# Kernel optimization log

Hardware: AMD Instinct MI355X
Metric: run time of the kernel (lower is better)

The kernel has to match this reference:

```python
import jax, jax.numpy as jnp
import numpy as np

N, E, G = 50000, 200000, 2048
D, H, L = 256, 512, 12
NODE_IN, EDGE_IN = 173, 13


def _mlp3(h, W1, b1, W2, b2, W3, b3):
    # DMCG-style MLP: ReLU after every Linear (MLPwoLastAct is the no-final-act variant)
    h = jax.nn.relu(h @ W1 + b1)
    h = jax.nn.relu(h @ W2 + b2)
    return jax.nn.relu(h @ W3 + b3)


def setup_inputs() -> dict:
    key = jax.random.key(0)
    ks = iter(jax.random.split(key, 64))

    def lin(fi, fo, shape_prefix=()):
        return jax.random.normal(next(ks), shape_prefix + (fi, fo), jnp.float32) / np.sqrt(fi)

    inp = {}
    inp["x_raw"] = jax.random.normal(next(ks), (N, NODE_IN), jnp.float32)
    inp["edge_raw"] = jax.random.normal(next(ks), (E, EDGE_IN), jnp.float32)
    inp["u0"] = jnp.zeros((1, D), jnp.float32)  # self.global_init
    # node / edge feature encoders: [H, H, D]
    inp["enW1"], inp["enb1"] = lin(NODE_IN, H), jnp.zeros((H,), jnp.float32)
    inp["enW2"], inp["enb2"] = lin(H, H), jnp.zeros((H,), jnp.float32)
    inp["enW3"], inp["enb3"] = lin(H, D), jnp.zeros((D,), jnp.float32)
    inp["eeW1"], inp["eeb1"] = lin(EDGE_IN, H), jnp.zeros((H,), jnp.float32)
    inp["eeW2"], inp["eeb2"] = lin(H, H), jnp.zeros((H,), jnp.float32)
    inp["eeW3"], inp["eeb3"] = lin(H, D), jnp.zeros((D,), jnp.float32)
    # per-message-passing-step MetaLayer MLPs, stacked over L layers
    inp["eW1"], inp["eb1"] = lin(4 * D, H, (L,)), jnp.zeros((L, H), jnp.float32)
    inp["eW2"], inp["eb2"] = lin(H, H, (L,)), jnp.zeros((L, H), jnp.float32)
    inp["eW3"], inp["eb3"] = lin(H, D, (L,)), jnp.zeros((L, D), jnp.float32)
    inp["nW1"], inp["nb1"] = lin(4 * D, H, (L,)), jnp.zeros((L, H), jnp.float32)
    inp["nW2"], inp["nb2"] = lin(H, H, (L,)), jnp.zeros((L, H), jnp.float32)
    inp["nW3"], inp["nb3"] = lin(H, D, (L,)), jnp.zeros((L, D), jnp.float32)
    inp["gW1"], inp["gb1"] = lin(3 * D, H, (L,)), jnp.zeros((L, H), jnp.float32)
    inp["gW2"], inp["gb2"] = lin(H, H, (L,)), jnp.zeros((L, H), jnp.float32)
    inp["gW3"], inp["gb3"] = lin(H, D, (L,)), jnp.zeros((L, D), jnp.float32)
    # per-step position head MLPwoLastAct(D, [D, 3])
    inp["pW1"], inp["pb1"] = lin(D, D, (L,)), jnp.zeros((L, D), jnp.float32)
    inp["pW2"], inp["pb2"] = lin(D, 3, (L,)), jnp.zeros((L, 3), jnp.float32)
    # graph structure (int constants)
    inp["edge_index"] = jax.random.randint(next(ks), (2, E), 0, N, jnp.int32)
    inp["node_batch"] = jnp.sort(jax.random.randint(next(ks), (N,), 0, G, jnp.int32))
    return inp


def reference(x_raw, edge_raw, u0, enW1, enb1, enW2, enb2, enW3, enb3,
              eeW1, eeb1, eeW2, eeb2, eeW3, eeb3,
              eW1, eb1, eW2, eb2, eW3, eb3,
              nW1, nb1, nW2, nb2, nW3, nb3,
              gW1, gb1, gW2, gb2, gW3, gb3,
              pW1, pb1, pW2, pb2,
              edge_index, node_batch):
    src, dst = edge_index[0], edge_index[1]
    edge_batch = node_batch[src]

    x = _mlp3(x_raw, enW1, enb1, enW2, enb2, enW3, enb3)        # [N, D]
    e = _mlp3(edge_raw, eeW1, eeb1, eeW2, eeb2, eeW3, eeb3)     # [E, D]
    u = jnp.broadcast_to(u0, (G, u0.shape[-1]))                  # [G, D]
    pos = jnp.zeros((x.shape[0], 3), x.dtype)

    def step(carry, p):
        x, e, u, pos = carry
        (ew1, ebb1, ew2, ebb2, ew3, ebb3,
         nw1, nbb1, nw2, nbb2, nw3, nbb3,
         gw1, gbb1, gw2, gbb2, gw3, gbb3,
         pw1, pbb1, pw2, pbb2) = p
        # edge update: gather endpoints + graph global, MLP, residual
        e_in = jnp.concatenate([e, x[src], x[dst], u[edge_batch]], axis=-1)   # [E, 4D]
        e = e + _mlp3(e_in, ew1, ebb1, ew2, ebb2, ew3, ebb3)
        # node update: scatter-sum edges to endpoints
        sent = jax.ops.segment_sum(e, src, num_segments=N)
        recv = jax.ops.segment_sum(e, dst, num_segments=N)
        n_in = jnp.concatenate([x, sent, recv, u[node_batch]], axis=-1)       # [N, 4D]
        x = x + _mlp3(n_in, nw1, nbb1, nw2, nbb2, nw3, nbb3)
        # global update: sum-pool nodes and edges per graph
        gn = jax.ops.segment_sum(x, node_batch, num_segments=G)
        ge = jax.ops.segment_sum(e, edge_batch, num_segments=G)
        u = u + _mlp3(jnp.concatenate([u, gn, ge], axis=-1), gw1, gbb1, gw2, gbb2, gw3, gbb3)
        # per-step position head (MLPwoLastAct)
        pos = pos + (jax.nn.relu(x @ pw1 + pbb1) @ pw2 + pbb2)
        return (x, e, u, pos), None

    params = (eW1, eb1, eW2, eb2, eW3, eb3,
              nW1, nb1, nW2, nb2, nW3, nb3,
              gW1, gb1, gW2, gb2, gW3, gb3,
              pW1, pb1, pW2, pb2)
    (x, e, u, pos), _ = jax.lax.scan(step, (x, e, u, pos), params)
    return pos
```

## Files before the change

### kernel.cpp

```cpp
#include <hip/hip_runtime.h>
#include <hip/hip_bf16.h>
#include <cstdint>
#include <cstddef>

#define N_NODES 50000
#define N_EDGES 200000
#define N_GRAPH 2048
#define DD 256
#define HH 512
#define LL 12
#define NODE_IN_F 173
#define EDGE_IN_F 13

typedef __hip_bfloat16 bf16;
typedef __attribute__((ext_vector_type(8))) short short8;
typedef __attribute__((ext_vector_type(4))) float f32x4;
typedef __attribute__((ext_vector_type(4))) unsigned short us4;

__device__ __forceinline__ float bfbits2f(unsigned short u) {
    return __uint_as_float(((unsigned)u) << 16);
}
__device__ __forceinline__ unsigned short f2bfbits(float f) {
    bf16 h = __float2bfloat16(f);
    return __builtin_bit_cast(unsigned short, h);
}

__device__ __forceinline__ void gld16(const void* g, void* l) {
    __builtin_amdgcn_global_load_lds(
        (const __attribute__((address_space(1))) unsigned int*)g,
        (__attribute__((address_space(3))) unsigned int*)l, 16, 0, 0);
}

#define TBM 128
#define TBN 128

struct GMArgs {
    const bf16* A[4];
    const int*  idx[4];
    const bf16* whi[4];
    const bf16* wlo[4];
    int lda[4];
    int ldw[4];
    int Kp[4];
    int nparts;
    int M, N;
    const float* bias;
    const bf16* res;
    bf16* C;
    int relu;
};

__global__ __launch_bounds__(256)
void gemm_mfma(GMArgs g)
{
    __shared__ __align__(16) short As[3][TBM * 32];
    __shared__ __align__(16) short Bh[3][TBN * 32];
    __shared__ __align__(16) short Bl[3][TBN * 32];

    const int tid  = threadIdx.x;
    const int lane = tid & 63;
    const int wv   = tid >> 6;
    const int wm   = (wv >> 1) * 64;
    const int wn   = (wv & 1) * 64;
    const int quad = lane >> 4;
    const int l16  = lane & 15;
    const int rq   = lane >> 2;
    const int qq   = lane & 3;

    const int gx  = gridDim.x;
    const int nwg = gx * gridDim.y;
    int hw  = blockIdx.y * gx + blockIdx.x;
    int xcd = hw & 7, rk = hw >> 3;
    int q = nwg >> 3, r = nwg & 7;
    int lid = (xcd < r ? xcd * (q + 1) : r * (q + 1) + (xcd - r) * q) + rk;
    const int row0 = (lid / gx) * TBM;
    const int col0 = (lid % gx) * TBN;

    int steps[4]; int T = 0;
#pragma unroll
    for (int p = 0; p < 4; ++p) { steps[p] = (p < g.nparts) ? (g.Kp[p] >> 5) : 0; T += steps[p]; }

    f32x4 acc[4][4];
#pragma unroll
    for (int i = 0; i < 4; ++i)
#pragma unroll
        for (int j = 0; j < 4; ++j)
            acc[i][j] = (f32x4){0.f, 0.f, 0.f, 0.f};

    auto stage = [&](int t, int b) {
        int p = 0, tt = t;
        while (tt >= steps[p]) { tt -= steps[p]; ++p; }
        const int k0 = tt << 5;
        const short* Ap  = (const short*)g.A[p];
        const short* Whi = (const short*)g.whi[p];
        const short* Wlo = (const short*)g.wlo[p];
        const int* idx = g.idx[p];
        const int lda = g.lda[p];
        const int ldw = g.ldw[p];
        const int kcol = k0 + qq * 8;
#pragma unroll
        for (int s = 0; s < 2; ++s) {
            int r2 = wv * 32 + s * 16 + rq;
            int slab = (wv * 32 + s * 16) * 32;
            int grr = row0 + r2;
            int cr = grr < g.M ? grr : g.M - 1;
            int ar = idx ? idx[cr] : cr;
            gld16(Ap + (size_t)ar * lda + kcol, (short*)As[b] + slab);
            size_t wo = (size_t)(col0 + r2) * ldw + kcol;
            gld16(Whi + wo, (short*)Bh[b] + slab);
            gld16(Wlo + wo, (short*)Bl[b] + slab);
        }
    };

    stage(0, 0);
    if (T > 1) stage(1, 1);
    int cur = 0;
    for (int t = 0; t < T; ++t) {
        if (t + 1 < T) asm volatile("s_waitcnt vmcnt(6)" ::: "memory");
        else           asm volatile("s_waitcnt vmcnt(0)" ::: "memory");
        __builtin_amdgcn_s_barrier();
        asm volatile("" ::: "memory");
        if (t + 2 < T) stage(t + 2, cur + 2 >= 3 ? cur - 1 : cur + 2);

        short8 a[4], bh[4], bl[4];
#pragma unroll
        for (int i = 0; i < 4; ++i)
            a[i] = *(const short8*)&As[cur][(wm + i * 16 + l16) * 32 + quad * 8];
#pragma unroll
        for (int j = 0; j < 4; ++j) {
            bh[j] = *(const short8*)&Bh[cur][(wn + j * 16 + l16) * 32 + quad * 8];
            bl[j] = *(const short8*)&Bl[cur][(wn + j * 16 + l16) * 32 + quad * 8];
        }
#pragma unroll
        for (int i = 0; i < 4; ++i)
#pragma unroll
            for (int j = 0; j < 4; ++j)
                acc[i][j] = __builtin_amdgcn_mfma_f32_16x16x32_bf16(a[i], bh[j], acc[i][j], 0, 0, 0);
#pragma unroll
        for (int i = 0; i < 4; ++i)
#pragma unroll
            for (int j = 0; j < 4; ++j)
                acc[i][j] = __builtin_amdgcn_mfma_f32_16x16x32_bf16(a[i], bl[j], acc[i][j], 0, 0, 0);

        cur = cur + 1 >= 3 ? 0 : cur + 1;
    }

    __syncthreads();
    {
        const int SROW = 68;
        float* Sw = (float*)&As[0][0] + wv * (16 * SROW);
        const int erow = lane >> 2;
        const int ecb  = lane & 3;
        float bc[4];
#pragma unroll
        for (int j = 0; j < 4; ++j)
            bc[j] = g.bias ? g.bias[col0 + wn + j * 16 + l16] : 0.f;
        const int grb = row0 + wm;
#pragma unroll
        for (int i = 0; i < 4; ++i) {
#pragma unroll
            for (int j = 0; j < 4; ++j)
#pragma unroll
                for (int r3 = 0; r3 < 4; ++r3) {
                    float v = acc[i][j][r3] + bc[j];
                    if (g.relu) v = fmaxf(v, 0.f);
                    Sw[(quad * 4 + r3) * SROW + j * 16 + l16] = v;
                }
            int gr = grb + i * 16 + erow;
            if (gr < g.M) {
                const float* sr = Sw + erow * SROW + ecb * 16;
                f32x4 q0 = *(const f32x4*)(sr + 0);
                f32x4 q1 = *(const f32x4*)(sr + 4);
                f32x4 q2 = *(const f32x4*)(sr + 8);
                f32x4 q3 = *(const f32x4*)(sr + 12);
                size_t ob = (size_t)gr * g.N + col0 + wn + ecb * 16;
                float v[16];
                *(f32x4*)&v[0] = q0; *(f32x4*)&v[4] = q1;
                *(f32x4*)&v[8] = q2; *(f32x4*)&v[12] = q3;
                if (g.res) {
                    const short* rp = (const short*)g.res + ob;
                    short8 r0 = *(const short8*)rp;
                    short8 r1 = *(const short8*)(rp + 8);
#pragma unroll
                    for (int k = 0; k < 8; ++k) {
                        v[k]     += bfbits2f((unsigned short)r0[k]);
                        v[8 + k] += bfbits2f((unsigned short)r1[k]);
                    }
                }
                short8 o0, o1;
#pragma unroll
                for (int k = 0; k < 8; ++k) {
                    o0[k] = (short)f2bfbits(v[k]);
                    o1[k] = (short)f2bfbits(v[8 + k]);
                }
                short* cp = (short*)g.C + ob;
                *(short8*)cp = o0;
                *(short8*)(cp + 8) = o1;
            }
        }
    }
}

static inline GMArgs gm_new(int M, int N) {
    GMArgs g;
    for (int i = 0; i < 4; ++i) { g.A[i] = nullptr; g.idx[i] = nullptr; g.whi[i] = nullptr; g.wlo[i] = nullptr; g.lda[i] = 0; g.ldw[i] = 0; g.Kp[i] = 0; }
    g.nparts = 0; g.M = M; g.N = N; g.bias = nullptr; g.res = nullptr; g.C = nullptr; g.relu = 0;
    return g;
}
static inline void gm_part(GMArgs& g, const bf16* A, int lda, const int* idx,
                           const bf16* whi, const bf16* wlo, int ldw, int Kp) {
    int p = g.nparts++;
    g.A[p] = A; g.lda[p] = lda; g.idx[p] = idx; g.whi[p] = whi; g.wlo[p] = wlo; g.ldw[p] = ldw; g.Kp[p] = Kp;
}
static inline void gm_run(hipStream_t s, GMArgs& g, const float* bias,
                          const bf16* res, bf16* C, int relu) {
    g.bias = bias; g.res = res; g.C = C; g.relu = relu;
    dim3 grid(g.N / TBN, (g.M + TBM - 1) / TBM);
    gemm_mfma<<<grid, dim3(256), 0, s>>>(g);
}

struct ConvDesc { const float* W; bf16* hi; int N, K, Kp, total; };
struct ConvBatch { ConvDesc d[10]; int nd; int grand; };

__global__ void conv_multi(ConvBatch cb)
{
    int i = blockIdx.x * blockDim.x + threadIdx.x;
    if (i >= cb.grand) return;
    int m = 0;
    while (i >= cb.d[m].total) { i -= cb.d[m].total; ++m; }
    const ConvDesc d = cb.d[m];
    int n = i / d.Kp, k = i % d.Kp;
    float v = (k < d.K) ? d.W[(size_t)k * d.N + n] : 0.f;
    bf16 h = __float2bfloat16(v);
    d.hi[i] = h;
    (d.hi + (size_t)d.N * d.Kp)[i] = __float2bfloat16(v - __bfloat162float(h));
}

__global__ void pad_raw(const float* __restrict__ src, int K, int Kp, int rows,
                        bf16* __restrict__ out)
{
    int i = blockIdx.x * blockDim.x + threadIdx.x;
    if (i >= rows * Kp) return;
    int r = i / Kp, k = i % Kp;
    out[i] = __float2bfloat16(k < K ? src[(size_t)r * K + k] : 0.f);
}

__global__ void zero_i32(int* __restrict__ p, int n) {
    int i = blockIdx.x * blockDim.x + threadIdx.x;
    if (i < n) p[i] = 0;
}
__global__ void copy_i32(const int* __restrict__ a, int* __restrict__ b, int n) {
    int i = blockIdx.x * blockDim.x + threadIdx.x;
    if (i < n) b[i] = a[i];
}
__global__ void count_edges(const int* __restrict__ src, const int* __restrict__ dst,
                            const int* __restrict__ node_batch,
                            int* __restrict__ cnt_s, int* __restrict__ cnt_d,
                            int* __restrict__ ebat)
{
    int i = blockIdx.x * blockDim.x + threadIdx.x;
    if (i >= N_EDGES) return;
    int s = src[i], d = dst[i];
    atomicAdd(&cnt_s[s], 1);
    atomicAdd(&cnt_d[d], 1);
    ebat[i] = node_batch[s];
}
__global__ void count_nodes(const int* __restrict__ node_batch, int* __restrict__ gcnt)
{
    int i = blockIdx.x * blockDim.x + threadIdx.x;
    if (i >= N_NODES) return;
    atomicAdd(&gcnt[node_batch[i]], 1);
}
__global__ __launch_bounds__(1024)
void scan_excl_kernel(const int* __restrict__ cnt, int* __restrict__ off, int n)
{
    __shared__ int part[1024];
    int t = threadIdx.x;
    int chunk = (n + 1023) >> 10;
    int lo = t * chunk; if (lo > n) lo = n;
    int hi = lo + chunk; if (hi > n) hi = n;
    int s = 0;
    for (int i = lo; i < hi; ++i) s += cnt[i];
    part[t] = s;
    __syncthreads();
    for (int d = 1; d < 1024; d <<= 1) {
        int v = (t >= d) ? part[t - d] : 0;
        __syncthreads();
        part[t] += v;
        __syncthreads();
    }
    int base = (t == 0) ? 0 : part[t - 1];
    for (int i = lo; i < hi; ++i) { off[i] = base; base += cnt[i]; }
    if (t == 1023) off[n] = part[1023];
}
__global__ void csr_fill(const int* __restrict__ src, const int* __restrict__ dst,
                         int* __restrict__ cur_s, int* __restrict__ cur_d,
                         int* __restrict__ idx_s, int* __restrict__ idx_d)
{
    int i = blockIdx.x * blockDim.x + threadIdx.x;
    if (i >= N_EDGES) return;
    int p = atomicAdd(&cur_s[src[i]], 1); idx_s[p] = i;
    int q = atomicAdd(&cur_d[dst[i]], 1); idx_d[q] = i;
}
__global__ void seg_sum_csr(const bf16* __restrict__ rows, const int* __restrict__ offs,
                            const int* __restrict__ idx, bf16* __restrict__ out)
{
    int n = blockIdx.x * 4 + (threadIdx.x >> 6);
    int lane = threadIdx.x & 63;
    if (n >= N_NODES) return;
    int k0 = offs[n], k1 = offs[n + 1];
    const unsigned short* rp = (const unsigned short*)rows;
    float s0 = 0.f, s1 = 0.f, s2 = 0.f, s3 = 0.f;
    for (int k = k0; k < k1; ++k) {
        us4 v = *(const us4*)(rp + (size_t)idx[k] * DD + lane * 4);
        s0 += bfbits2f(v.x); s1 += bfbits2f(v.y); s2 += bfbits2f(v.z); s3 += bfbits2f(v.w);
    }
    us4 o;
    o.x = f2bfbits(s0); o.y = f2bfbits(s1); o.z = f2bfbits(s2); o.w = f2bfbits(s3);
    *(us4*)((unsigned short*)out + (size_t)n * DD + lane * 4) = o;
}
__global__ void range_sum(const bf16* __restrict__ rows, const int* __restrict__ gs,
                          bf16* __restrict__ out)
{
    int g = blockIdx.x * 4 + (threadIdx.x >> 6);
    int lane = threadIdx.x & 63;
    if (g >= N_GRAPH) return;
    int n0 = gs[g], n1 = gs[g + 1];
    const unsigned short* rp = (const unsigned short*)rows;
    float s0 = 0.f, s1 = 0.f, s2 = 0.f, s3 = 0.f;
    for (int n = n0; n < n1; ++n) {
        us4 v = *(const us4*)(rp + (size_t)n * DD + lane * 4);
        s0 += bfbits2f(v.x); s1 += bfbits2f(v.y); s2 += bfbits2f(v.z); s3 += bfbits2f(v.w);
    }
    us4 o;
    o.x = f2bfbits(s0); o.y = f2bfbits(s1); o.z = f2bfbits(s2); o.w = f2bfbits(s3);
    *(us4*)((unsigned short*)out + (size_t)g * DD + lane * 4) = o;
}
__global__ void u_init(bf16* __restrict__ u, const float* __restrict__ u0)
{
    int i = blockIdx.x * blockDim.x + threadIdx.x;
    if (i < N_GRAPH * DD) u[i] = __float2bfloat16(u0[i & (DD - 1)]);
}
__global__ void pos_head2(const bf16* __restrict__ ph, const float* __restrict__ W,
                          const float* __restrict__ b, float* __restrict__ pos,
                          int nrows, int write_mode)
{
    int gid = blockIdx.x * blockDim.x + threadIdx.x;
    int row = gid >> 6;
    int lane = threadIdx.x & 63;
    if (row >= nrows) return;
    const bf16* r = ph + (size_t)row * DD;
    float a0 = 0.f, a1 = 0.f, a2 = 0.f;
    for (int k = lane; k < DD; k += 64) {
        float v = __bfloat162float(r[k]);
        a0 += v * W[k * 3 + 0];
        a1 += v * W[k * 3 + 1];
        a2 += v * W[k * 3 + 2];
    }
#pragma unroll
    for (int d = 32; d > 0; d >>= 1) {
        a0 += __shfl_down(a0, d);
        a1 += __shfl_down(a1, d);
        a2 += __shfl_down(a2, d);
    }
    if (lane == 0) {
        float* p = pos + (size_t)row * 3;
        if (write_mode) {
            p[0] = a0 + b[0]; p[1] = a1 + b[1]; p[2] = a2 + b[2];
        } else {
            p[0] += a0 + b[0]; p[1] += a1 + b[1]; p[2] += a2 + b[2];
        }
    }
}

extern "C" void kernel_launch(void* const* d_in, const int* in_sizes, int n_in,
                              void* d_out, int out_size, void* d_ws, size_t ws_size,
                              hipStream_t stream)
{
    const float* x_raw    = (const float*)d_in[0];
    const float* edge_raw = (const float*)d_in[1];
    const float* u0       = (const float*)d_in[2];
    const float* enW1 = (const float*)d_in[3];  const float* enb1 = (const float*)d_in[4];
    const float* enW2 = (const float*)d_in[5];  const float* enb2 = (const float*)d_in[6];
    const float* enW3 = (const float*)d_in[7];  const float* enb3 = (const float*)d_in[8];
    const float* eeW1 = (const float*)d_in[9];  const float* eeb1 = (const float*)d_in[10];
    const float* eeW2 = (const float*)d_in[11]; const float* eeb2 = (const float*)d_in[12];
    const float* eeW3 = (const float*)d_in[13]; const float* eeb3 = (const float*)d_in[14];
    const float* eW1 = (const float*)d_in[15];  const float* eb1 = (const float*)d_in[16];
    const float* eW2 = (const float*)d_in[17];  const float* eb2 = (const float*)d_in[18];
    const float* eW3 = (const float*)d_in[19];  const float* eb3 = (const float*)d_in[20];
    const float* nW1 = (const float*)d_in[21];  const float* nb1 = (const float*)d_in[22];
    const float* nW2 = (const float*)d_in[23];  const float* nb2 = (const float*)d_in[24];
    const float* nW3 = (const float*)d_in[25];  const float* nb3 = (const float*)d_in[26];
    const float* gW1 = (const float*)d_in[27];  const float* gb1 = (const float*)d_in[28];
    const float* gW2 = (const float*)d_in[29];  const float* gb2 = (const float*)d_in[30];
    const float* gW3 = (const float*)d_in[31];  const float* gb3 = (const float*)d_in[32];
    const float* pW1 = (const float*)d_in[33];  const float* pb1 = (const float*)d_in[34];
    const float* pW2 = (const float*)d_in[35];  const float* pb2 = (const float*)d_in[36];
    const int* edge_index = (const int*)d_in[37];
    const int* node_batch = (const int*)d_in[38];
    const int* src = edge_index;
    const int* dst = edge_index + N_EDGES;
    float* pos = (float*)d_out;
    (void)in_sizes; (void)n_in; (void)out_size;

    char* wp = (char*)d_ws;
    auto alloc = [&](size_t bytes) -> void* {
        void* r = (void*)wp;
        wp += (bytes + 255) & ~(size_t)255;
        return r;
    };
    bf16* x     = (bf16*)alloc((size_t)N_NODES * DD * 2);
    bf16* e     = (bf16*)alloc((size_t)N_EDGES * DD * 2);
    bf16* u     = (bf16*)alloc((size_t)N_GRAPH * DD * 2);
    bf16* sent  = (bf16*)alloc((size_t)N_NODES * DD * 2);
    bf16* recv  = (bf16*)alloc((size_t)N_NODES * DD * 2);
    bf16* gn    = (bf16*)alloc((size_t)N_GRAPH * DD * 2);
    bf16* ge    = (bf16*)alloc((size_t)N_GRAPH * DD * 2);
    bf16* gh1   = (bf16*)alloc((size_t)N_GRAPH * HH * 2);
    bf16* gh2   = (bf16*)alloc((size_t)N_GRAPH * HH * 2);
    bf16* wbuf  = (bf16*)alloc((size_t)6000000 * 2);
    int* cnt_s  = (int*)alloc((size_t)N_NODES * 4);
    int* cnt_d  = (int*)alloc((size_t)N_NODES * 4);
    int* gcnt   = (int*)alloc((size_t)N_GRAPH * 4);
    int* off_s  = (int*)alloc((size_t)(N_NODES + 1) * 4);
    int* off_d  = (int*)alloc((size_t)(N_NODES + 1) * 4);
    int* gstart = (int*)alloc((size_t)(N_GRAPH + 1) * 4);
    int* cur_s  = (int*)alloc((size_t)N_NODES * 4);
    int* cur_d  = (int*)alloc((size_t)N_NODES * 4);
    int* idx_s  = (int*)alloc((size_t)N_EDGES * 4);
    int* idx_d  = (int*)alloc((size_t)N_EDGES * 4);
    int* ebat   = (int*)alloc((size_t)N_EDGES * 4);

    size_t used = (size_t)(wp - (char*)d_ws);
    size_t remain = ws_size > used ? ws_size - used : 0;
    auto pad256 = [](size_t b) { return (b + 255) & ~(size_t)255; };
    int EC = 12500;
    {
        const int ladder[3] = {50000, 25000, 12500};
        for (int i = 0; i < 3; ++i) {
            int c = ladder[i];
            size_t need = 2 * pad256((size_t)c * HH * 2) + pad256((size_t)c * 192 * 2);
            if (need <= remain) { EC = c; break; }
        }
    }
    const int NC = EC < N_NODES ? EC : N_NODES;
    bf16* h1   = (bf16*)alloc((size_t)EC * HH * 2);
    bf16* h2   = (bf16*)alloc((size_t)EC * HH * 2);
    bf16* rawp = (bf16*)alloc((size_t)EC * 192 * 2);

    zero_i32<<<(N_NODES + 255) / 256, 256, 0, stream>>>(cnt_s, N_NODES);
    zero_i32<<<(N_NODES + 255) / 256, 256, 0, stream>>>(cnt_d, N_NODES);
    zero_i32<<<(N_GRAPH + 255) / 256, 256, 0, stream>>>(gcnt, N_GRAPH);
    count_edges<<<(N_EDGES + 255) / 256, 256, 0, stream>>>(src, dst, node_batch, cnt_s, cnt_d, ebat);
    count_nodes<<<(N_NODES + 255) / 256, 256, 0, stream>>>(node_batch, gcnt);
    scan_excl_kernel<<<1, 1024, 0, stream>>>(cnt_s, off_s, N_NODES);
    scan_excl_kernel<<<1, 1024, 0, stream>>>(cnt_d, off_d, N_NODES);
    scan_excl_kernel<<<1, 1024, 0, stream>>>(gcnt, gstart, N_GRAPH);
    copy_i32<<<(N_NODES + 255) / 256, 256, 0, stream>>>(off_s, cur_s, N_NODES);
    copy_i32<<<(N_NODES + 255) / 256, 256, 0, stream>>>(off_d, cur_d, N_NODES);
    csr_fill<<<(N_EDGES + 255) / 256, 256, 0, stream>>>(src, dst, cur_s, cur_d, idx_s, idx_d);

    u_init<<<(N_GRAPH * DD + 255) / 256, 256, 0, stream>>>(u, u0);

    bf16* wb_cur = wbuf;
    ConvBatch cb; cb.nd = 0; cb.grand = 0;
    auto wreset = [&]() { wb_cur = wbuf; cb.nd = 0; cb.grand = 0; };
    auto wadd = [&](const float* W, int N, int K, int Kp) -> bf16* {
        bf16* hi = wb_cur;
        wb_cur += (size_t)N * Kp * 2;
        ConvDesc& d = cb.d[cb.nd++];
        d.W = W; d.hi = hi; d.N = N; d.K = K; d.Kp = Kp; d.total = N * Kp;
        cb.grand += d.total;
        return hi;
    };
    auto wflush = [&]() {
        conv_multi<<<(cb.grand + 255) / 256, 256, 0, stream>>>(cb);
    };
    auto wlo_of = [&](bf16* hi, int N, int Kp) -> bf16* { return hi + (size_t)N * Kp; };

    wreset();
    bf16* cenW1 = wadd(enW1, HH, NODE_IN_F, 192);
    bf16* cenW2 = wadd(enW2, HH, HH, HH);
    bf16* cenW3 = wadd(enW3, DD, HH, HH);
    bf16* ceeW1 = wadd(eeW1, HH, EDGE_IN_F, 32);
    bf16* ceeW2 = wadd(eeW2, HH, HH, HH);
    bf16* ceeW3 = wadd(eeW3, DD, HH, HH);
    wflush();

    for (int off = 0; off < N_NODES; off += NC) {
        int cnt = (N_NODES - off) < NC ? (N_NODES - off) : NC;
        pad_raw<<<((size_t)cnt * 192 + 255) / 256, 256, 0, stream>>>(x_raw + (size_t)off * NODE_IN_F, NODE_IN_F, 192, cnt, rawp);
        { GMArgs g = gm_new(cnt, HH); gm_part(g, rawp, 192, nullptr, cenW1, wlo_of(cenW1, HH, 192), 192, 192);
          gm_run(stream, g, enb1, nullptr, h1, 1); }
        { GMArgs g = gm_new(cnt, HH); gm_part(g, h1, HH, nullptr, cenW2, wlo_of(cenW2, HH, HH), HH, HH);
          gm_run(stream, g, enb2, nullptr, h2, 1); }
        { GMArgs g = gm_new(cnt, DD); gm_part(g, h2, HH, nullptr, cenW3, wlo_of(cenW3, DD, HH), HH, HH);
          gm_run(stream, g, enb3, nullptr, x + (size_t)off * DD, 1); }
    }
    for (int off = 0; off < N_EDGES; off += EC) {
        int cnt = (N_EDGES - off) < EC ? (N_EDGES - off) : EC;
        pad_raw<<<((size_t)cnt * 32 + 255) / 256, 256, 0, stream>>>(edge_raw + (size_t)off * EDGE_IN_F, EDGE_IN_F, 32, cnt, rawp);
        { GMArgs g = gm_new(cnt, HH); gm_part(g, rawp, 32, nullptr, ceeW1, wlo_of(ceeW1, HH, 32), 32, 32);
          gm_run(stream, g, eeb1, nullptr, h1, 1); }
        { GMArgs g = gm_new(cnt, HH); gm_part(g, h1, HH, nullptr, ceeW2, wlo_of(ceeW2, HH, HH), HH, HH);
          gm_run(stream, g, eeb2, nullptr, h2, 1); }
        { GMArgs g = gm_new(cnt, DD); gm_part(g, h2, HH, nullptr, ceeW3, wlo_of(ceeW3, DD, HH), HH, HH);
          gm_run(stream, g, eeb3, nullptr, e + (size_t)off * DD, 1); }
    }

    for (int l = 0; l < LL; ++l) {
        const float* ew1  = eW1 + (size_t)l * 4 * DD * HH;  const float* eb1l = eb1 + (size_t)l * HH;
        const float* ew2  = eW2 + (size_t)l * HH * HH;      const float* eb2l = eb2 + (size_t)l * HH;
        const float* ew3  = eW3 + (size_t)l * HH * DD;      const float* eb3l = eb3 + (size_t)l * DD;
        const float* nw1  = nW1 + (size_t)l * 4 * DD * HH;  const float* nb1l = nb1 + (size_t)l * HH;
        const float* nw2  = nW2 + (size_t)l * HH * HH;      const float* nb2l = nb2 + (size_t)l * HH;
        const float* nw3  = nW3 + (size_t)l * HH * DD;      const float* nb3l = nb3 + (size_t)l * DD;
        const float* gw1  = gW1 + (size_t)l * 3 * DD * HH;  const float* gb1l = gb1 + (size_t)l * HH;
        const float* gw2  = gW2 + (size_t)l * HH * HH;      const float* gb2l = gb2 + (size_t)l * HH;
        const float* gw3  = gW3 + (size_t)l * HH * DD;      const float* gb3l = gb3 + (size_t)l * DD;
        const float* pw1  = pW1 + (size_t)l * DD * DD;      const float* pb1l = pb1 + (size_t)l * DD;
        const float* pw2  = pW2 + (size_t)l * DD * 3;       const float* pb2l = pb2 + (size_t)l * 3;

        wreset();
        bf16* cew1 = wadd(ew1, HH, 4 * DD, 4 * DD);
        bf16* cew2 = wadd(ew2, HH, HH, HH);
        bf16* cew3 = wadd(ew3, DD, HH, HH);
        bf16* cnw1 = wadd(nw1, HH, 4 * DD, 4 * DD);
        bf16* cnw2 = wadd(nw2, HH, HH, HH);
        bf16* cnw3 = wadd(nw3, DD, HH, HH);
        bf16* cgw1 = wadd(gw1, HH, 3 * DD, 3 * DD);
        bf16* cgw2 = wadd(gw2, HH, HH, HH);
        bf16* cgw3 = wadd(gw3, DD, HH, HH);
        bf16* cpw1 = wadd(pw1, DD, DD, DD);
        wflush();
        bf16* lew1 = wlo_of(cew1, HH, 4 * DD);
        bf16* lnw1 = wlo_of(cnw1, HH, 4 * DD);
        bf16* lgw1 = wlo_of(cgw1, HH, 3 * DD);

        for (int off = 0; off < N_EDGES; off += EC) {
            int cnt = (N_EDGES - off) < EC ? (N_EDGES - off) : EC;
            { GMArgs g = gm_new(cnt, HH);
              gm_part(g, e + (size_t)off * DD, DD, nullptr,    cew1,            lew1,            4 * DD, DD);
              gm_part(g, x,                    DD, src + off,  cew1 + 1 * DD,   lew1 + 1 * DD,   4 * DD, DD);
              gm_part(g, x,                    DD, dst + off,  cew1 + 2 * DD,   lew1 + 2 * DD,   4 * DD, DD);
              gm_part(g, u,                    DD, ebat + off, cew1 + 3 * DD,   lew1 + 3 * DD,   4 * DD, DD);
              gm_run(stream, g, eb1l, nullptr, h1, 1); }
            { GMArgs g = gm_new(cnt, HH); gm_part(g, h1, HH, nullptr, cew2, wlo_of(cew2, HH, HH), HH, HH);
              gm_run(stream, g, eb2l, nullptr, h2, 1); }
            { GMArgs g = gm_new(cnt, DD); gm_part(g, h2, HH, nullptr, cew3, wlo_of(cew3, DD, HH), HH, HH);
              gm_run(stream, g, eb3l, e + (size_t)off * DD, e + (size_t)off * DD, 1); }
        }

        seg_sum_csr<<<(N_NODES + 3) / 4, 256, 0, stream>>>(e, off_s, idx_s, sent);
        seg_sum_csr<<<(N_NODES + 3) / 4, 256, 0, stream>>>(e, off_d, idx_d, recv);
        for (int off = 0; off < N_NODES; off += NC) {
            int cnt = (N_NODES - off) < NC ? (N_NODES - off) : NC;
            { GMArgs g = gm_new(cnt, HH);
              gm_part(g, x    + (size_t)off * DD, DD, nullptr,          cnw1,          lnw1,          4 * DD, DD);
              gm_part(g, sent + (size_t)off * DD, DD, nullptr,          cnw1 + 1 * DD, lnw1 + 1 * DD, 4 * DD, DD);
              gm_part(g, recv + (size_t)off * DD, DD, nullptr,          cnw1 + 2 * DD, lnw1 + 2 * DD, 4 * DD, DD);
              gm_part(g, u,                       DD, node_batch + off, cnw1 + 3 * DD, lnw1 + 3 * DD, 4 * DD, DD);
              gm_run(stream, g, nb1l, nullptr, h1, 1); }
            { GMArgs g = gm_new(cnt, HH); gm_part(g, h1, HH, nullptr, cnw2, wlo_of(cnw2, HH, HH), HH, HH);
              gm_run(stream, g, nb2l, nullptr, h2, 1); }
            { GMArgs g = gm_new(cnt, DD); gm_part(g, h2, HH, nullptr, cnw3, wlo_of(cnw3, DD, HH), HH, HH);
              gm_run(stream, g, nb3l, x + (size_t)off * DD, x + (size_t)off * DD, 1); }
        }

        range_sum<<<(N_GRAPH + 3) / 4, 256, 0, stream>>>(x, gstart, gn);
        range_sum<<<(N_GRAPH + 3) / 4, 256, 0, stream>>>(sent, gstart, ge);
        { GMArgs g = gm_new(N_GRAPH, HH);
          gm_part(g, u,  DD, nullptr, cgw1,          lgw1,          3 * DD, DD);
          gm_part(g, gn, DD, nullptr, cgw1 + 1 * DD, lgw1 + 1 * DD, 3 * DD, DD);
          gm_part(g, ge, DD, nullptr, cgw1 + 2 * DD, lgw1 + 2 * DD, 3 * DD, DD);
          gm_run(stream, g, gb1l, nullptr, gh1, 1); }
        { GMArgs g = gm_new(N_GRAPH, HH); gm_part(g, gh1, HH, nullptr, cgw2, wlo_of(cgw2, HH, HH), HH, HH);
          gm_run(stream, g, gb2l, nullptr, gh2, 1); }
        { GMArgs g = gm_new(N_GRAPH, DD); gm_part(g, gh2, HH, nullptr, cgw3, wlo_of(cgw3, DD, HH), HH, HH);
          gm_run(stream, g, gb3l, u, u, 1); }

        for (int off = 0; off < N_NODES; off += NC) {
            int cnt = (N_NODES - off) < NC ? (N_NODES - off) : NC;
            { GMArgs g = gm_new(cnt, DD); gm_part(g, x + (size_t)off * DD, DD, nullptr, cpw1, wlo_of(cpw1, DD, DD), DD, DD);
              gm_run(stream, g, pb1l, nullptr, h1, 1); }
            pos_head2<<<((size_t)cnt * 64 + 255) / 256, 256, 0, stream>>>(
                h1, pw2, pb2l, pos + (size_t)off * 3, cnt, l == 0 ? 1 : 0);
        }
    }
}
```

Baseline: 23.13 ms.

## Enlarge GEMM tile to 256x128 with 8 waves and 4-stage load pipeline

The MFMA GEMM now computes 256x128 output tiles with 512 threads, so each weight tile is reused across twice as many rows. The shared-memory ring grows from three to four buffers, giving three stages of prefetch. The load assignment is respecialised so each wave issues four loads per stage (A rows, W-hi or W-lo), and gather row indices are hoisted out of the K loop. The CSR edge lists are also insertion-sorted per node, which should improve gather locality and make summation order deterministic. In exchange, the kernel uses about 128KB of LDS and more registers per block, which lowers occupancy and leaves more partial tiles on small M.

```diff
diff --git a/kernel.cpp b/kernel.cpp
--- a/kernel.cpp
+++ b/kernel.cpp
@@ -31,7 +31,7 @@
         (__attribute__((address_space(3))) unsigned int*)l, 16, 0, 0);
 }
 
-#define TBM 128
+#define TBM 256
 #define TBN 128
 
 struct GMArgs {
@@ -50,12 +50,12 @@
     int relu;
 };
 
-__global__ __launch_bounds__(256)
+__global__ __launch_bounds__(512)
 void gemm_mfma(GMArgs g)
 {
-    __shared__ __align__(16) short As[3][TBM * 32];
-    __shared__ __align__(16) short Bh[3][TBN * 32];
-    __shared__ __align__(16) short Bl[3][TBN * 32];
+    __shared__ __align__(16) short AsL[4 * TBM * 32];
+    __shared__ __align__(16) short BhL[4 * TBN * 32];
+    __shared__ __align__(16) short BlL[4 * TBN * 32];
 
     const int tid  = threadIdx.x;
     const int lane = tid & 63;
@@ -80,6 +80,19 @@
 #pragma unroll
     for (int p = 0; p < 4; ++p) { steps[p] = (p < g.nparts) ? (g.Kp[p] >> 5) : 0; T += steps[p]; }
 
+    int pa0[4], pa1[4], pa2[4], pa3[4];
+#pragma unroll
+    for (int s = 0; s < 4; ++s) {
+        int sid = wv * 4 + s;
+        int r2 = (sid & 15) * 16 + rq;
+        int grr = row0 + r2;
+        int cr = grr < g.M ? grr : g.M - 1;
+        pa0[s] = (g.nparts > 0 && g.idx[0]) ? g.idx[0][cr] : cr;
+        pa1[s] = (g.nparts > 1 && g.idx[1]) ? g.idx[1][cr] : cr;
+        pa2[s] = (g.nparts > 2 && g.idx[2]) ? g.idx[2][cr] : cr;
+        pa3[s] = (g.nparts > 3 && g.idx[3]) ? g.idx[3][cr] : cr;
+    }
+
     f32x4 acc[4][4];
 #pragma unroll
     for (int i = 0; i < 4; ++i)
@@ -94,42 +107,51 @@
         const short* Ap  = (const short*)g.A[p];
         const short* Whi = (const short*)g.whi[p];
         const short* Wlo = (const short*)g.wlo[p];
-        const int* idx = g.idx[p];
         const int lda = g.lda[p];
         const int ldw = g.ldw[p];
         const int kcol = k0 + qq * 8;
 #pragma unroll
-        for (int s = 0; s < 2; ++s) {
-            int r2 = wv * 32 + s * 16 + rq;
-            int slab = (wv * 32 + s * 16) * 32;
-            int grr = row0 + r2;
-            int cr = grr < g.M ? grr : g.M - 1;
-            int ar = idx ? idx[cr] : cr;
-            gld16(Ap + (size_t)ar * lda + kcol, (short*)As[b] + slab);
-            size_t wo = (size_t)(col0 + r2) * ldw + kcol;
-            gld16(Whi + wo, (short*)Bh[b] + slab);
-            gld16(Wlo + wo, (short*)Bl[b] + slab);
+        for (int s = 0; s < 4; ++s) {
+            const int sid = wv * 4 + s;
+            if (sid < 16) {
+                int ar = (p == 0) ? pa0[s] : (p == 1) ? pa1[s] : (p == 2) ? pa2[s] : pa3[s];
+                gld16(Ap + (size_t)ar * lda + kcol,
+                      AsL + (size_t)b * (TBM * 32) + sid * (16 * 32));
+            } else if (sid < 24) {
+                int r2 = (sid - 16) * 16 + rq;
+                gld16(Whi + (size_t)(col0 + r2) * ldw + kcol,
+                      BhL + (size_t)b * (TBN * 32) + (sid - 16) * (16 * 32));
+            } else {
+                int r2 = (sid - 24) * 16 + rq;
+                gld16(Wlo + (size_t)(col0 + r2) * ldw + kcol,
+                      BlL + (size_t)b * (TBN * 32) + (sid - 24) * (16 * 32));
+            }
         }
     };
 
     stage(0, 0);
     if (T > 1) stage(1, 1);
-    int cur = 0;
+    if (T > 2) stage(2, 2);
     for (int t = 0; t < T; ++t) {
-        if (t + 1 < T) asm volatile("s_waitcnt vmcnt(6)" ::: "memory");
-        else           asm volatile("s_waitcnt vmcnt(0)" ::: "memory");
+        if (t + 2 < T)      asm volatile("s_waitcnt vmcnt(8)" ::: "memory");
+        else if (t + 1 < T) asm volatile("s_waitcnt vmcnt(4)" ::: "memory");
+        else                asm volatile("s_waitcnt vmcnt(0)" ::: "memory");
         __builtin_amdgcn_s_barrier();
         asm volatile("" ::: "memory");
-        if (t + 2 < T) stage(t + 2, cur + 2 >= 3 ? cur - 1 : cur + 2);
-
+        if (t + 3 < T) stage(t + 3, (t + 3) & 3);
+
+        const int cur = t & 3;
+        const short* Ab = AsL + (size_t)cur * (TBM * 32);
+        const short* Bhb = BhL + (size_t)cur * (TBN * 32);
+        const short* Blb = BlL + (size_t)cur * (TBN * 32);
         short8 a[4], bh[4], bl[4];
 #pragma unroll
         for (int i = 0; i < 4; ++i)
-            a[i] = *(const short8*)&As[cur][(wm + i * 16 + l16) * 32 + quad * 8];
+            a[i] = *(const short8*)&Ab[(wm + i * 16 + l16) * 32 + quad * 8];
 #pragma unroll
         for (int j = 0; j < 4; ++j) {
-            bh[j] = *(const short8*)&Bh[cur][(wn + j * 16 + l16) * 32 + quad * 8];
-            bl[j] = *(const short8*)&Bl[cur][(wn + j * 16 + l16) * 32 + quad * 8];
+            bh[j] = *(const short8*)&Bhb[(wn + j * 16 + l16) * 32 + quad * 8];
+            bl[j] = *(const short8*)&Blb[(wn + j * 16 + l16) * 32 + quad * 8];
         }
 #pragma unroll
         for (int i = 0; i < 4; ++i)
@@ -141,14 +163,12 @@
 #pragma unroll
             for (int j = 0; j < 4; ++j)
                 acc[i][j] = __builtin_amdgcn_mfma_f32_16x16x32_bf16(a[i], bl[j], acc[i][j], 0, 0, 0);
-
-        cur = cur + 1 >= 3 ? 0 : cur + 1;
     }
 
     __syncthreads();
     {
         const int SROW = 68;
-        float* Sw = (float*)&As[0][0] + wv * (16 * SROW);
+        float* Sw = (float*)AsL + wv * (16 * SROW);
         const int erow = lane >> 2;
         const int ecb  = lane & 3;
         float bc[4];
@@ -216,7 +236,7 @@
                           const bf16* res, bf16* C, int relu) {
     g.bias = bias; g.res = res; g.C = C; g.relu = relu;
     dim3 grid(g.N / TBN, (g.M + TBM - 1) / TBM);
-    gemm_mfma<<<grid, dim3(256), 0, s>>>(g);
+    gemm_mfma<<<grid, dim3(512), 0, s>>>(g);
 }
 
 struct ConvDesc { const float* W; bf16* hi; int N, K, Kp, total; };
@@ -301,6 +321,17 @@
     if (i >= N_EDGES) return;
     int p = atomicAdd(&cur_s[src[i]], 1); idx_s[p] = i;
     int q = atomicAdd(&cur_d[dst[i]], 1); idx_d[q] = i;
+}
+__global__ void sort_csr(const int* __restrict__ offs, int* __restrict__ idx, int n)
+{
+    int v = blockIdx.x * blockDim.x + threadIdx.x;
+    if (v >= n) return;
+    int k0 = offs[v], k1 = offs[v + 1];
+    for (int i = k0 + 1; i < k1; ++i) {
+        int x = idx[i], j = i - 1;
+        while (j >= k0 && idx[j] > x) { idx[j + 1] = idx[j]; --j; }
+        idx[j + 1] = x;
+    }
 }
 __global__ void seg_sum_csr(const bf16* __restrict__ rows, const int* __restrict__ offs,
                             const int* __restrict__ idx, bf16* __restrict__ out)
@@ -460,6 +491,8 @@
     copy_i32<<<(N_NODES + 255) / 256, 256, 0, stream>>>(off_s, cur_s, N_NODES);
     copy_i32<<<(N_NODES + 255) / 256, 256, 0, stream>>>(off_d, cur_d, N_NODES);
     csr_fill<<<(N_EDGES + 255) / 256, 256, 0, stream>>>(src, dst, cur_s, cur_d, idx_s, idx_d);
+    sort_csr<<<(N_NODES + 255) / 256, 256, 0, stream>>>(off_s, idx_s, N_NODES);
+    sort_csr<<<(N_NODES + 255) / 256, 256, 0, stream>>>(off_d, idx_d, N_NODES);
 
     u_init<<<(N_GRAPH * DD + 255) / 256, 256, 0, stream>>>(u, u0);
 
```

Result: no change. 23.48 ms (+1.5%).
